# Kernel tuning notes

Measured on AMD Instinct MI355X. Metric: run time of the kernel, lower is better.

The kernel has to match this reference:

```python
import jax, jax.numpy as jnp
import numpy as np
import math

N_EMBD = 512
N_BRANCH = 4
BLOCK = 2048
B, T = 2, 2048


def make_rope_tables(dim, max_len):
    inv_freq = 1.0 / (10000.0 ** (np.arange(0, dim, 2, dtype=np.float32) / dim))
    t = np.arange(max_len, dtype=np.float32)
    freqs = np.einsum('i,j->ij', t, inv_freq)  # [max_len, dim/2]
    return jnp.asarray(np.cos(freqs)), jnp.asarray(np.sin(freqs))


def apply_rope(xq, cos, sin):
    # xq: [..., T, C]; cos/sin: [T, C/2]
    x1 = xq[..., 0::2]
    x2 = xq[..., 1::2]
    y1 = x1 * cos - x2 * sin
    y2 = x1 * sin + x2 * cos
    return jnp.stack((y1, y2), axis=-1).reshape(xq.shape)


def setup_inputs() -> dict:
    key = jax.random.key(0)
    ks = jax.random.split(key, 6)
    C, NB = N_EMBD, N_BRANCH
    s = 1.0 / math.sqrt(C)
    a = jax.random.normal(ks[0], (B, T, C), jnp.float32)
    x = jax.random.normal(ks[1], (B, T, C), jnp.float32)
    Wq = jax.random.normal(ks[2], (C, C * NB), jnp.float32) * s
    Wk = jax.random.normal(ks[3], (C, C), jnp.float32) * s
    Wv = jax.random.normal(ks[4], (C, C * NB), jnp.float32) * s
    Wo = jax.random.normal(ks[5], (C, C), jnp.float32) * s
    cos, sin = make_rope_tables(C, BLOCK)
    return {"a": a, "x": x, "Wq": Wq, "Wk": Wk, "Wv": Wv, "Wo": Wo,
            "cos": cos, "sin": sin}


def reference(a, x, Wq, Wk, Wv, Wo, cos, sin):
    Bb, Tt, C = x.shape
    NB = Wq.shape[1] // C
    cos_t = cos[:Tt]
    sin_t = sin[:Tt]

    q = (a @ Wq).reshape(Bb, Tt, NB, C).transpose(0, 2, 1, 3)  # [B,NB,T,C]
    v = (a @ Wv).reshape(Bb, Tt, NB, C).transpose(0, 2, 1, 3)  # [B,NB,T,C]
    k = (x @ Wk)[:, None, :, :]                                # [B,1,T,C]

    q = apply_rope(q, cos_t, sin_t)
    k = apply_rope(k, cos_t, sin_t)

    att = jnp.einsum('bntc,bosc->bnts', q, k) / math.sqrt(C)   # [B,NB,T,T]
    causal = jnp.tril(jnp.ones((Tt, Tt), bool))                # [T,T]
    att_m = jnp.where(causal, att, -jnp.inf)

    # softmax over branch axis; mask is identical across branches, so compute
    # on unmasked logits and zero-out masked positions (== nan_to_num of
    # softmax over fully -inf columns)
    soft_probs = jnp.where(causal, jax.nn.softmax(att, axis=1), 0.0)

    max_val = jnp.max(soft_probs, axis=1, keepdims=True)
    hard_mask = jax.lax.stop_gradient((soft_probs == max_val).astype(att.dtype))
    route_mask = jax.lax.stop_gradient(hard_mask - soft_probs) + soft_probs

    att_max = jnp.max(att_m, axis=1)                           # [B,T,T]
    attn_probs = jax.nn.softmax(att_max, axis=-1)              # [B,T,T]

    combined = attn_probs[:, None, :, :] * route_mask          # [B,NB,T,T]
    y = jnp.einsum('bnts,bnsc->btc', combined, v)              # [B,T,C]
    return y @ Wo
```

## Files before the change

kernel.cpp:

```cpp
#include <hip/hip_runtime.h>
#include <math.h>


#define B_ 2
#define T_ 2048
#define C_ 512
#define NB_ 4
#define C2_ 1024

typedef unsigned short u16;
typedef unsigned char u8;
using short8 = __attribute__((ext_vector_type(8))) short;
using bf16x8 = __attribute__((ext_vector_type(8))) __bf16;
using f32x4  = __attribute__((ext_vector_type(4))) float;

__device__ __forceinline__ float bf2f(u16 u) {
  union { unsigned int i; float f; } v; v.i = ((unsigned int)u) << 16; return v.f;
}
__device__ __forceinline__ u16 f2bf(float f) {
  union { float f; unsigned int i; } v; v.f = f;
  unsigned int u = v.i;
  return (u16)((u + 0x7fffu + ((u >> 16) & 1u)) >> 16);
}
__device__ __forceinline__ f32x4 mfma16x16x32(short8 a, short8 b, f32x4 c) {
  return __builtin_amdgcn_mfma_f32_16x16x32_bf16(
      __builtin_bit_cast(bf16x8, a), __builtin_bit_cast(bf16x8, b), c, 0, 0, 0);
}
__device__ __forceinline__ void split8(const float* s, uint4& hi, uint4& lo) {
  u16 h[8], l[8];
#pragma unroll
  for (int j = 0; j < 8; ++j) {
    h[j] = f2bf(s[j]);
    l[j] = f2bf(s[j] - bf2f(h[j]));
  }
  hi.x = h[0] | ((unsigned)h[1] << 16); hi.y = h[2] | ((unsigned)h[3] << 16);
  hi.z = h[4] | ((unsigned)h[5] << 16); hi.w = h[6] | ((unsigned)h[7] << 16);
  lo.x = l[0] | ((unsigned)l[1] << 16); lo.y = l[2] | ((unsigned)l[3] << 16);
  lo.z = l[4] | ((unsigned)l[5] << 16); lo.w = l[6] | ((unsigned)l[7] << 16);
}
__device__ __forceinline__ int swz(int row) { return ((row >> 1) & 3) << 3; }

template <int MODE>
__global__ __launch_bounds__(256) void gemm_qk(const float* __restrict__ A,
                                               const float* __restrict__ W,
                                               u16* __restrict__ out,
                                               const float* __restrict__ cosT,
                                               const float* __restrict__ sinT,
                                               const int N, const int K) {
  __shared__ u16 Ah[64][32], Al[64][32];
  __shared__ u16 Bh[64][32], Bl[64][32];
  const int tid = threadIdx.x;
  const int wave = tid >> 6, lane = tid & 63;
  const int m0 = blockIdx.y << 6, n0 = blockIdx.x << 6;
  const f32x4 zero = {0.f, 0.f, 0.f, 0.f};
  f32x4 acc[4] = {zero, zero, zero, zero};
  const int srow = tid >> 2, koff = ((tid & 3) << 3) ^ swz(tid >> 2);
  const int lrow = lane & 15, lk = ((lane >> 4) << 3) ^ swz(lane & 15);
  for (int kk = 0; kk < K; kk += 32) {
    const int kg = (tid & 3) << 3;
    float av[8];
    *(float4*)(av) = *(const float4*)(&A[(size_t)(m0 + srow) * K + kk + kg]);
    *(float4*)(av + 4) =
        *(const float4*)(&A[(size_t)(m0 + srow) * K + kk + kg + 4]);
    uint4 hi, lo;
    split8(av, hi, lo);
    *(uint4*)(&Ah[srow][koff]) = hi;
    *(uint4*)(&Al[srow][koff]) = lo;
    float wv[8];
#pragma unroll
    for (int j = 0; j < 8; ++j)
      wv[j] = W[(size_t)(kk + kg + j) * N + n0 + srow];
    split8(wv, hi, lo);
    *(uint4*)(&Bh[srow][koff]) = hi;
    *(uint4*)(&Bl[srow][koff]) = lo;
    __syncthreads();
    short8 ah = *(const short8*)(&Ah[(wave << 4) + lrow][lk]);
    short8 al = *(const short8*)(&Al[(wave << 4) + lrow][lk]);
#pragma unroll
    for (int ns = 0; ns < 4; ++ns) {
      short8 bh = *(const short8*)(&Bh[(ns << 4) + lrow][lk]);
      short8 bl = *(const short8*)(&Bl[(ns << 4) + lrow][lk]);
      acc[ns] = mfma16x16x32(ah, bh, acc[ns]);
      acc[ns] = mfma16x16x32(al, bh, acc[ns]);
      acc[ns] = mfma16x16x32(ah, bl, acc[ns]);
    }
    __syncthreads();
  }
  const int r0 = m0 + (wave << 4) + ((lane >> 4) << 2);
  const int cb = n0 + (lane & 15);
#pragma unroll
  for (int ns = 0; ns < 4; ++ns) {
#pragma unroll
    for (int r = 0; r < 4; ++r) {
      const int rg = r0 + r;
      const int cg = cb + (ns << 4);
      float v = acc[ns][r];
      float pv = __shfl_xor(v, 1);
      const int t = rg & (T_ - 1);
      const int c = (MODE == 1) ? (cg & (C_ - 1)) : cg;
      const int i = c >> 1;
      const float cf = cosT[(t << 8) + i];
      const float sf = sinT[(t << 8) + i];
      float x1 = (lane & 1) ? pv : v;
      float x2 = (lane & 1) ? v : pv;
      float y = (lane & 1) ? (x1 * sf + x2 * cf) : (x1 * cf - x2 * sf);
      if (MODE == 1) y *= 0.044194173824159216f;
      const u16 hi = f2bf(y);
      const u16 lo = f2bf(y - bf2f(hi));
      size_t rowoff;
      if (MODE == 1) {
        const int b = rg >> 11, n = cg >> 9;
        rowoff = ((size_t)((b * NB_ + n) * T_ + t)) * C2_;
      } else {
        rowoff = (size_t)rg * C2_;
      }
      out[rowoff + c] = hi;
      out[rowoff + C_ + c] = lo;
    }
  }
}

template <int AF32, int OF32>
__global__ __launch_bounds__(256) void gemm_hi(const void* __restrict__ Ap,
                                               const float* __restrict__ W,
                                               void* __restrict__ outp,
                                               const int N, const int K) {
  __shared__ u16 As[64][32];
  __shared__ u16 Bs[64][32];
  const int tid = threadIdx.x;
  const int wave = tid >> 6, lane = tid & 63;
  const int m0 = blockIdx.y << 6, n0 = blockIdx.x << 6;
  const f32x4 zero = {0.f, 0.f, 0.f, 0.f};
  f32x4 acc[4] = {zero, zero, zero, zero};
  const int srow = tid >> 2, koff = ((tid & 3) << 3) ^ swz(tid >> 2);
  const int lrow = lane & 15, lk = ((lane >> 4) << 3) ^ swz(lane & 15);
  for (int kk = 0; kk < K; kk += 32) {
    const int kg = (tid & 3) << 3;
    if (AF32) {
      const float* A = (const float*)Ap;
      float av[8];
      *(float4*)(av) = *(const float4*)(&A[(size_t)(m0 + srow) * K + kk + kg]);
      *(float4*)(av + 4) =
          *(const float4*)(&A[(size_t)(m0 + srow) * K + kk + kg + 4]);
      uint4 hi;
      hi.x = f2bf(av[0]) | ((unsigned)f2bf(av[1]) << 16);
      hi.y = f2bf(av[2]) | ((unsigned)f2bf(av[3]) << 16);
      hi.z = f2bf(av[4]) | ((unsigned)f2bf(av[5]) << 16);
      hi.w = f2bf(av[6]) | ((unsigned)f2bf(av[7]) << 16);
      *(uint4*)(&As[srow][koff]) = hi;
    } else {
      const u16* A = (const u16*)Ap;
      *(uint4*)(&As[srow][koff]) =
          *(const uint4*)(&A[(size_t)(m0 + srow) * K + kk + kg]);
    }
    uint4 hi;
    {
      float w[8];
#pragma unroll
      for (int j = 0; j < 8; ++j)
        w[j] = W[(size_t)(kk + kg + j) * N + n0 + srow];
      hi.x = f2bf(w[0]) | ((unsigned)f2bf(w[1]) << 16);
      hi.y = f2bf(w[2]) | ((unsigned)f2bf(w[3]) << 16);
      hi.z = f2bf(w[4]) | ((unsigned)f2bf(w[5]) << 16);
      hi.w = f2bf(w[6]) | ((unsigned)f2bf(w[7]) << 16);
    }
    *(uint4*)(&Bs[srow][koff]) = hi;
    __syncthreads();
    short8 af = *(const short8*)(&As[(wave << 4) + lrow][lk]);
#pragma unroll
    for (int ns = 0; ns < 4; ++ns) {
      short8 bf = *(const short8*)(&Bs[(ns << 4) + lrow][lk]);
      acc[ns] = mfma16x16x32(af, bf, acc[ns]);
    }
    __syncthreads();
  }
  const int r0 = m0 + (wave << 4) + ((lane >> 4) << 2);
  const int cb = n0 + (lane & 15);
#pragma unroll
  for (int ns = 0; ns < 4; ++ns) {
#pragma unroll
    for (int r = 0; r < 4; ++r) {
      const size_t idx = (size_t)(r0 + r) * N + cb + (ns << 4);
      if (OF32) ((float*)outp)[idx] = acc[ns][r];
      else ((u16*)outp)[idx] = f2bf(acc[ns][r]);
    }
  }
}

__global__ __launch_bounds__(256) void transpose_v_k(const u16* __restrict__ Vraw,
                                                     u16* __restrict__ VT) {
  const int bid = blockIdx.x;
  const int ct = bid & 7;
  const int ttile = (bid >> 3) & 31;
  const int n = (bid >> 8) & 3;
  const int b = bid >> 10;
  __shared__ u16 tile[64][68];
  const int tid = threadIdx.x;
  const int rr = tid >> 4;
  const int cc = (tid & 15) << 2;
  const int t0 = ttile << 6, c0 = ct << 6;
#pragma unroll
  for (int it = 0; it < 4; ++it) {
    const int r = (it << 4) + rr;
    *(ushort4*)(&tile[r][cc]) = *(const ushort4*)(
        &Vraw[((size_t)((b << 11) + t0 + r)) * (NB_ * C_) + n * C_ + c0 + cc]);
  }
  __syncthreads();
#pragma unroll
  for (int it = 0; it < 4; ++it) {
    const int c = (it << 4) + rr;
    ushort4 w;
    w.x = tile[cc + 0][c]; w.y = tile[cc + 1][c];
    w.z = tile[cc + 2][c]; w.w = tile[cc + 3][c];
    *(ushort4*)(&VT[((size_t)((b * NB_ + n) * C_ + c0 + c)) * T_ + t0 + cc]) = w;
  }
}

__global__ __launch_bounds__(256) void scores_k(const u16* __restrict__ Qcat,
                                                const u16* __restrict__ Kcat,
                                                u16* __restrict__ Mout,
                                                u8* __restrict__ Mask) {
  const int tri = blockIdx.x;
  int tt = (int)((sqrtf(8.f * (float)tri + 1.f) - 1.f) * 0.5f);
  while ((tt + 1) * (tt + 2) / 2 <= tri) ++tt;
  while (tt * (tt + 1) / 2 > tri) --tt;
  const int ss = tri - tt * (tt + 1) / 2;
  const int b = blockIdx.y;
  __shared__ u16 Qh[NB_][64][32], Ql[NB_][64][32];
  __shared__ u16 Kh[64][32], Kl[64][32];
  const int tid = threadIdx.x;
  const int wave = tid >> 6, lane = tid & 63;
  const int t0 = tt << 6, s0 = ss << 6;
  const f32x4 zero = {0.f, 0.f, 0.f, 0.f};
  f32x4 acc[NB_][4];
  for (int n = 0; n < NB_; ++n)
    for (int j = 0; j < 4; ++j) acc[n][j] = zero;
  const int srow = tid >> 2, koff = ((tid & 3) << 3) ^ swz(tid >> 2);
  const int lrow = lane & 15, lk = ((lane >> 4) << 3) ^ swz(lane & 15);
  const int kg = (tid & 3) << 3;
  for (int kk = 0; kk < C_; kk += 32) {
#pragma unroll
    for (int n = 0; n < NB_; ++n) {
      const size_t qb =
          ((size_t)((b * NB_ + n) * T_ + t0 + srow)) * C2_ + kk + kg;
      *(uint4*)(&Qh[n][srow][koff]) = *(const uint4*)(&Qcat[qb]);
      *(uint4*)(&Ql[n][srow][koff]) = *(const uint4*)(&Qcat[qb + C_]);
    }
    const size_t kb = ((size_t)((b << 11) + s0 + srow)) * C2_ + kk + kg;
    *(uint4*)(&Kh[srow][koff]) = *(const uint4*)(&Kcat[kb]);
    *(uint4*)(&Kl[srow][koff]) = *(const uint4*)(&Kcat[kb + C_]);
    __syncthreads();
    short8 qh[NB_], ql[NB_];
#pragma unroll
    for (int n = 0; n < NB_; ++n) {
      qh[n] = *(const short8*)(&Qh[n][(wave << 4) + lrow][lk]);
      ql[n] = *(const short8*)(&Ql[n][(wave << 4) + lrow][lk]);
    }
#pragma unroll
    for (int ns = 0; ns < 4; ++ns) {
      short8 kh = *(const short8*)(&Kh[(ns << 4) + lrow][lk]);
      short8 kl = *(const short8*)(&Kl[(ns << 4) + lrow][lk]);
#pragma unroll
      for (int n = 0; n < NB_; ++n) {
        acc[n][ns] = mfma16x16x32(qh[n], kh, acc[n][ns]);
        acc[n][ns] = mfma16x16x32(ql[n], kh, acc[n][ns]);
        acc[n][ns] = mfma16x16x32(qh[n], kl, acc[n][ns]);
      }
    }
    __syncthreads();
  }
  const int tb = t0 + (wave << 4) + ((lane >> 4) << 2);
  const int sb = s0 + (lane & 15);
#pragma unroll
  for (int ns = 0; ns < 4; ++ns) {
#pragma unroll
    for (int r = 0; r < 4; ++r) {
      const int t = tb + r, s = sb + (ns << 4);
      float a0 = acc[0][ns][r], a1 = acc[1][ns][r];
      float a2 = acc[2][ns][r], a3 = acc[3][ns][r];
      float m = fmaxf(fmaxf(a0, a1), fmaxf(a2, a3));
      u8 msk = (u8)((a0 == m) | ((a1 == m) << 1) | ((a2 == m) << 2) |
                    ((a3 == m) << 3));
      if (s > t) { m = -__builtin_inff(); msk = 0; }
      const size_t idx = (size_t)b * T_ * T_ + (size_t)t * T_ + s;
      Mout[idx] = f2bf(m);
      Mask[idx] = msk;
    }
  }
}

__global__ __launch_bounds__(256) void rowstats_k(const u16* __restrict__ Mb,
                                                  float* __restrict__ Rm,
                                                  float* __restrict__ Rz) {
  const int r = (blockIdx.x << 2) + (threadIdx.x >> 6);
  const int lane = threadIdx.x & 63;
  const int b = r >> 11, t = r & (T_ - 1);
  const u16* row = Mb + (size_t)b * T_ * T_ + (size_t)t * T_;
  float m = -__builtin_inff();
  for (int s = lane; s <= t; s += 64) m = fmaxf(m, bf2f(row[s]));
#pragma unroll
  for (int off = 32; off; off >>= 1) m = fmaxf(m, __shfl_xor(m, off));
  float z = 0.f;
  for (int s = lane; s <= t; s += 64) z += expf(bf2f(row[s]) - m);
#pragma unroll
  for (int off = 32; off; off >>= 1) z += __shfl_xor(z, off);
  if (lane == 0) { Rm[r] = m; Rz[r] = 1.f / z; }
}

__global__ __launch_bounds__(256) void pbuild_k(const u16* __restrict__ Mb,
                                                const float* __restrict__ Rm,
                                                const float* __restrict__ Rz,
                                                u16* __restrict__ Pb) {
  const int r = blockIdx.x;
  const float rm = Rm[r], rz = Rz[r];
  const size_t off = ((size_t)r << 11) + (threadIdx.x << 3);
  ushort4 m0 = *(const ushort4*)(&Mb[off]);
  ushort4 m1 = *(const ushort4*)(&Mb[off + 4]);
  u16 o[8];
  o[0] = f2bf(expf(bf2f(m0.x) - rm) * rz);
  o[1] = f2bf(expf(bf2f(m0.y) - rm) * rz);
  o[2] = f2bf(expf(bf2f(m0.z) - rm) * rz);
  o[3] = f2bf(expf(bf2f(m0.w) - rm) * rz);
  o[4] = f2bf(expf(bf2f(m1.x) - rm) * rz);
  o[5] = f2bf(expf(bf2f(m1.y) - rm) * rz);
  o[6] = f2bf(expf(bf2f(m1.z) - rm) * rz);
  o[7] = f2bf(expf(bf2f(m1.w) - rm) * rz);
  uint4 w;
  w.x = o[0] | ((unsigned)o[1] << 16); w.y = o[2] | ((unsigned)o[3] << 16);
  w.z = o[4] | ((unsigned)o[5] << 16); w.w = o[6] | ((unsigned)o[7] << 16);
  *(uint4*)(&Pb[off]) = w;
}

__global__ __launch_bounds__(256) void pv_k(const u16* __restrict__ Pb,
                                            const u8* __restrict__ Mask,
                                            const u16* __restrict__ VT,
                                            u16* __restrict__ Y) {
  const int ypair = blockIdx.x, cblk = blockIdx.y, b = blockIdx.z;
  const int c0 = cblk << 5;
  __shared__ u16 Ps[NB_][64][32];
  __shared__ u16 Vs[NB_][32][32];
  const int tid = threadIdx.x;
  const int wave = tid >> 6, lane = tid & 63;
  const int prow = tid >> 2, soff = (tid & 3) << 3;
  const int psoff = soff ^ swz(prow);
  const int vrow = tid >> 3, vsoff = (tid & 7) << 2;
  const int vcol = ((((tid & 7) >> 1) ^ ((vrow >> 1) & 3)) << 3) |
                   ((tid & 1) << 2);
  const int lrow = lane & 15, lk = ((lane >> 4) << 3) ^ swz(lane & 15);
  const f32x4 zero = {0.f, 0.f, 0.f, 0.f};
  const size_t vrow_base[NB_] = {
      ((size_t)((b * NB_ + 0) * C_ + c0 + vrow)) * T_,
      ((size_t)((b * NB_ + 1) * C_ + c0 + vrow)) * T_,
      ((size_t)((b * NB_ + 2) * C_ + c0 + vrow)) * T_,
      ((size_t)((b * NB_ + 3) * C_ + c0 + vrow)) * T_};

  for (int half = 0; half < 2; ++half) {
    const int tt = half ? (31 - ypair) : ypair;
    const int t0 = tt << 6;
    const int nchunk = (tt + 1) << 1;
    const size_t pro = ((size_t)((b << 11) + t0 + prow)) << 11;
    f32x4 acc[2] = {zero, zero};
    uint4 pu; uint2 mk2; uint2 vv[NB_];
    pu = *(const uint4*)(&Pb[pro + soff]);
    mk2 = *(const uint2*)(&Mask[pro + soff]);
#pragma unroll
    for (int n = 0; n < NB_; ++n)
      vv[n] = *(const uint2*)(&VT[vrow_base[n] + vsoff]);
    for (int ck = 0; ck < nchunk; ++ck) {
      u16 p[8] = {(u16)pu.x, (u16)(pu.x >> 16), (u16)pu.y, (u16)(pu.y >> 16),
                  (u16)pu.z, (u16)(pu.z >> 16), (u16)pu.w, (u16)(pu.w >> 16)};
      u8 mk[8] = {(u8)mk2.x, (u8)(mk2.x >> 8), (u8)(mk2.x >> 16),
                  (u8)(mk2.x >> 24), (u8)mk2.y, (u8)(mk2.y >> 8),
                  (u8)(mk2.y >> 16), (u8)(mk2.y >> 24)};
#pragma unroll
      for (int n = 0; n < NB_; ++n) {
        uint4 wv;
        wv.x = (unsigned)(((mk[0] >> n) & 1) ? p[0] : 0) |
               ((unsigned)(((mk[1] >> n) & 1) ? p[1] : 0) << 16);
        wv.y = (unsigned)(((mk[2] >> n) & 1) ? p[2] : 0) |
               ((unsigned)(((mk[3] >> n) & 1) ? p[3] : 0) << 16);
        wv.z = (unsigned)(((mk[4] >> n) & 1) ? p[4] : 0) |
               ((unsigned)(((mk[5] >> n) & 1) ? p[5] : 0) << 16);
        wv.w = (unsigned)(((mk[6] >> n) & 1) ? p[6] : 0) |
               ((unsigned)(((mk[7] >> n) & 1) ? p[7] : 0) << 16);
        *(uint4*)(&Ps[n][prow][psoff]) = wv;
        *(uint2*)(&Vs[n][vrow][vcol]) = vv[n];
      }
      __syncthreads();
      if (ck + 1 < nchunk) {
        const int sB = (ck + 1) << 5;
        pu = *(const uint4*)(&Pb[pro + sB + soff]);
        mk2 = *(const uint2*)(&Mask[pro + sB + soff]);
#pragma unroll
        for (int n = 0; n < NB_; ++n)
          vv[n] = *(const uint2*)(&VT[vrow_base[n] + sB + vsoff]);
      }
#pragma unroll
      for (int n = 0; n < NB_; ++n) {
        short8 af = *(const short8*)(&Ps[n][(wave << 4) + lrow][lk]);
#pragma unroll
        for (int cs = 0; cs < 2; ++cs) {
          short8 bf = *(const short8*)(&Vs[n][(cs << 4) + lrow][lk]);
          acc[cs] = mfma16x16x32(af, bf, acc[cs]);
        }
      }
      __syncthreads();
    }
    const int tb = t0 + (wave << 4) + ((lane >> 4) << 2);
    const int cbs = c0 + (lane & 15);
#pragma unroll
    for (int cs = 0; cs < 2; ++cs) {
#pragma unroll
      for (int r = 0; r < 4; ++r) {
        Y[(size_t)((b << 11) + tb + r) * C_ + cbs + (cs << 4)] =
            f2bf(acc[cs][r]);
      }
    }
  }
}

extern "C" void kernel_launch(void* const* d_in, const int* in_sizes, int n_in,
                              void* d_out, int out_size, void* d_ws,
                              size_t ws_size, hipStream_t stream) {
  (void)in_sizes; (void)n_in; (void)out_size; (void)ws_size;
  const float* a    = (const float*)d_in[0];
  const float* x    = (const float*)d_in[1];
  const float* Wq   = (const float*)d_in[2];
  const float* Wk   = (const float*)d_in[3];
  const float* Wv   = (const float*)d_in[4];
  const float* Wo   = (const float*)d_in[5];
  const float* cosT = (const float*)d_in[6];
  const float* sinT = (const float*)d_in[7];

  char* w = (char*)d_ws;
  u16* Qcat   = (u16*)(w + 0);
  u16* Kcat   = (u16*)(w + 33554432);
  u16* Vraw   = (u16*)(w + 41943040);
  u16* VT     = (u16*)(w + 58720256);
  u8*  Mask   = (u8*)(w + 75497472);
  float* Rm   = (float*)(w + 83886080);
  float* Rz   = (float*)(w + 83902464);
  u16* Pb     = (u16*)(w + 83918848);
  u16* Mb     = Vraw;
  u16* Y      = Qcat;

  const dim3 blk(256);
  gemm_qk<1><<<dim3(32, 64), blk, 0, stream>>>(a, Wq, Qcat, cosT, sinT, 2048, 512);
  gemm_qk<2><<<dim3(8, 64), blk, 0, stream>>>(x, Wk, Kcat, cosT, sinT, 512, 512);
  gemm_hi<1, 0><<<dim3(32, 64), blk, 0, stream>>>(a, Wv, (void*)Vraw, 2048, 512);
  transpose_v_k<<<dim3(2048), blk, 0, stream>>>(Vraw, VT);
  scores_k<<<dim3(528, 2), blk, 0, stream>>>(Qcat, Kcat, Mb, Mask);
  rowstats_k<<<dim3(1024), blk, 0, stream>>>(Mb, Rm, Rz);
  pbuild_k<<<dim3(4096), blk, 0, stream>>>(Mb, Rm, Rz, Pb);
  pv_k<<<dim3(16, 16, 2), blk, 0, stream>>>(Pb, Mask, VT, Y);
  gemm_hi<0, 1><<<dim3(8, 64), blk, 0, stream>>>(Y, Wo, d_out, 512, 512);
}
```

Before: 393.8 us.

## Double-buffer scores_k LDS tiles with async global_load_lds prefetch

Replaces register-staged global-to-LDS copies in the scores kernel with direct global_load_lds transfers into double-buffered shared-memory tiles. The next K-slice is prefetched while the current one feeds the MFMAs, using explicit vmcnt waits and raw barriers. The XOR swizzle on LDS rows is dropped because the direct LDS load writes a fixed lane-contiguous layout, which can bring back LDS bank conflicts on the fragment reads. LDS use doubles, which may lower occupancy.

```diff
diff --git a/kernel.cpp b/kernel.cpp
--- a/kernel.cpp
+++ b/kernel.cpp
@@ -226,8 +226,8 @@
   while (tt * (tt + 1) / 2 > tri) --tt;
   const int ss = tri - tt * (tt + 1) / 2;
   const int b = blockIdx.y;
-  __shared__ u16 Qh[NB_][64][32], Ql[NB_][64][32];
-  __shared__ u16 Kh[64][32], Kl[64][32];
+  __shared__ __align__(16) u16 Qh[2][NB_][64][32], Ql[2][NB_][64][32];
+  __shared__ __align__(16) u16 Kh[2][64][32], Kl[2][64][32];
   const int tid = threadIdx.x;
   const int wave = tid >> 6, lane = tid & 63;
   const int t0 = tt << 6, s0 = ss << 6;
@@ -235,31 +235,55 @@
   f32x4 acc[NB_][4];
   for (int n = 0; n < NB_; ++n)
     for (int j = 0; j < 4; ++j) acc[n][j] = zero;
-  const int srow = tid >> 2, koff = ((tid & 3) << 3) ^ swz(tid >> 2);
-  const int lrow = lane & 15, lk = ((lane >> 4) << 3) ^ swz(lane & 15);
-  const int kg = (tid & 3) << 3;
+  const int srow = tid >> 2, kg = (tid & 3) << 3;
+  const int lrow = lane & 15, lk = (lane >> 4) << 3;
+  const int wrow = wave << 4;
+  const size_t qstride = (size_t)T_ * C2_;
+  const size_t qbase = ((size_t)(b * NB_ * T_ + t0 + srow)) * C2_ + kg;
+  const size_t kbase = ((size_t)((b << 11) + s0 + srow)) * C2_ + kg;
+
+  auto stage_sc = [&](int d, int kko) {
+#pragma unroll
+    for (int n = 0; n < NB_; ++n) {
+      const size_t qb = qbase + (size_t)n * qstride + kko;
+      __builtin_amdgcn_global_load_lds(
+          (const __attribute__((address_space(1))) void*)&Qcat[qb],
+          (__attribute__((address_space(3))) void*)&Qh[d][n][wrow][0], 16, 0, 0);
+      __builtin_amdgcn_global_load_lds(
+          (const __attribute__((address_space(1))) void*)&Qcat[qb + C_],
+          (__attribute__((address_space(3))) void*)&Ql[d][n][wrow][0], 16, 0, 0);
+    }
+    __builtin_amdgcn_global_load_lds(
+        (const __attribute__((address_space(1))) void*)&Kcat[kbase + kko],
+        (__attribute__((address_space(3))) void*)&Kh[d][wrow][0], 16, 0, 0);
+    __builtin_amdgcn_global_load_lds(
+        (const __attribute__((address_space(1))) void*)&Kcat[kbase + kko + C_],
+        (__attribute__((address_space(3))) void*)&Kl[d][wrow][0], 16, 0, 0);
+  };
+
+  stage_sc(0, 0);
+  int cur = 0;
+#pragma unroll 2
   for (int kk = 0; kk < C_; kk += 32) {
+    if (kk + 32 < C_) {
+      stage_sc(cur ^ 1, kk + 32);
+      asm volatile("s_waitcnt vmcnt(10)" ::: "memory");
+    } else {
+      asm volatile("s_waitcnt vmcnt(0)" ::: "memory");
+    }
+    __builtin_amdgcn_sched_barrier(0);
+    __builtin_amdgcn_s_barrier();
+    __builtin_amdgcn_sched_barrier(0);
+    short8 qh[NB_], ql[NB_];
 #pragma unroll
     for (int n = 0; n < NB_; ++n) {
-      const size_t qb =
-          ((size_t)((b * NB_ + n) * T_ + t0 + srow)) * C2_ + kk + kg;
-      *(uint4*)(&Qh[n][srow][koff]) = *(const uint4*)(&Qcat[qb]);
-      *(uint4*)(&Ql[n][srow][koff]) = *(const uint4*)(&Qcat[qb + C_]);
-    }
-    const size_t kb = ((size_t)((b << 11) + s0 + srow)) * C2_ + kk + kg;
-    *(uint4*)(&Kh[srow][koff]) = *(const uint4*)(&Kcat[kb]);
-    *(uint4*)(&Kl[srow][koff]) = *(const uint4*)(&Kcat[kb + C_]);
-    __syncthreads();
-    short8 qh[NB_], ql[NB_];
-#pragma unroll
-    for (int n = 0; n < NB_; ++n) {
-      qh[n] = *(const short8*)(&Qh[n][(wave << 4) + lrow][lk]);
-      ql[n] = *(const short8*)(&Ql[n][(wave << 4) + lrow][lk]);
+      qh[n] = *(const short8*)(&Qh[cur][n][wrow + lrow][lk]);
+      ql[n] = *(const short8*)(&Ql[cur][n][wrow + lrow][lk]);
     }
 #pragma unroll
     for (int ns = 0; ns < 4; ++ns) {
-      short8 kh = *(const short8*)(&Kh[(ns << 4) + lrow][lk]);
-      short8 kl = *(const short8*)(&Kl[(ns << 4) + lrow][lk]);
+      short8 kh = *(const short8*)(&Kh[cur][(ns << 4) + lrow][lk]);
+      short8 kl = *(const short8*)(&Kl[cur][(ns << 4) + lrow][lk]);
 #pragma unroll
       for (int n = 0; n < NB_; ++n) {
         acc[n][ns] = mfma16x16x32(qh[n], kh, acc[n][ns]);
@@ -267,7 +291,11 @@
         acc[n][ns] = mfma16x16x32(qh[n], kl, acc[n][ns]);
       }
     }
-    __syncthreads();
+    __builtin_amdgcn_sched_barrier(0);
+    asm volatile("" ::: "memory");
+    __builtin_amdgcn_s_barrier();
+    __builtin_amdgcn_sched_barrier(0);
+    cur ^= 1;
   }
   const int tb = t0 + (wave << 4) + ((lane >> 4) << 2);
   const int sb = s0 + (lane & 15);
```

Result: faster. 378.8 us (-3.8%).

## Fuse softmax probability build into PV kernel and remap score tile order

Applied to the files above, without the earlier changes.

Removes the separate pbuild_k pass by computing exp(m - rowmax) * rinv on the fly inside pv_k from the bf16 max-logit matrix and row stats. This avoids writing and rereading a full T×T bf16 probability buffer per batch and saves one launch. The cost is that the exps are recomputed redundantly across the 16 column blocks of pv_k. Separately, scores_k's block-to-triangle mapping is permuted (interleaving by 8 with stride 66) to spread heavy and light tiles across the scheduler.

```diff
diff --git a/kernel.cpp b/kernel.cpp
--- a/kernel.cpp
+++ b/kernel.cpp
@@ -220,7 +220,7 @@
                                                 const u16* __restrict__ Kcat,
                                                 u16* __restrict__ Mout,
                                                 u8* __restrict__ Mask) {
-  const int tri = blockIdx.x;
+  const int tri = ((blockIdx.x & 7) * 66) + (blockIdx.x >> 3);
   int tt = (int)((sqrtf(8.f * (float)tri + 1.f) - 1.f) * 0.5f);
   while ((tt + 1) * (tt + 2) / 2 <= tri) ++tt;
   while (tt * (tt + 1) / 2 > tri) --tt;
@@ -307,31 +307,9 @@
   if (lane == 0) { Rm[r] = m; Rz[r] = 1.f / z; }
 }
 
-__global__ __launch_bounds__(256) void pbuild_k(const u16* __restrict__ Mb,
-                                                const float* __restrict__ Rm,
-                                                const float* __restrict__ Rz,
-                                                u16* __restrict__ Pb) {
-  const int r = blockIdx.x;
-  const float rm = Rm[r], rz = Rz[r];
-  const size_t off = ((size_t)r << 11) + (threadIdx.x << 3);
-  ushort4 m0 = *(const ushort4*)(&Mb[off]);
-  ushort4 m1 = *(const ushort4*)(&Mb[off + 4]);
-  u16 o[8];
-  o[0] = f2bf(expf(bf2f(m0.x) - rm) * rz);
-  o[1] = f2bf(expf(bf2f(m0.y) - rm) * rz);
-  o[2] = f2bf(expf(bf2f(m0.z) - rm) * rz);
-  o[3] = f2bf(expf(bf2f(m0.w) - rm) * rz);
-  o[4] = f2bf(expf(bf2f(m1.x) - rm) * rz);
-  o[5] = f2bf(expf(bf2f(m1.y) - rm) * rz);
-  o[6] = f2bf(expf(bf2f(m1.z) - rm) * rz);
-  o[7] = f2bf(expf(bf2f(m1.w) - rm) * rz);
-  uint4 w;
-  w.x = o[0] | ((unsigned)o[1] << 16); w.y = o[2] | ((unsigned)o[3] << 16);
-  w.z = o[4] | ((unsigned)o[5] << 16); w.w = o[6] | ((unsigned)o[7] << 16);
-  *(uint4*)(&Pb[off]) = w;
-}
-
-__global__ __launch_bounds__(256) void pv_k(const u16* __restrict__ Pb,
+__global__ __launch_bounds__(256) void pv_k(const u16* __restrict__ Mb,
+                                            const float* __restrict__ Rm,
+                                            const float* __restrict__ Rz,
                                             const u8* __restrict__ Mask,
                                             const u16* __restrict__ VT,
                                             u16* __restrict__ Y) {
@@ -358,17 +336,23 @@
     const int tt = half ? (31 - ypair) : ypair;
     const int t0 = tt << 6;
     const int nchunk = (tt + 1) << 1;
-    const size_t pro = ((size_t)((b << 11) + t0 + prow)) << 11;
+    const int rg = (b << 11) + t0 + prow;
+    const size_t pro = (size_t)rg << 11;
+    const float rm = Rm[rg], rz = Rz[rg];
     f32x4 acc[2] = {zero, zero};
     uint4 pu; uint2 mk2; uint2 vv[NB_];
-    pu = *(const uint4*)(&Pb[pro + soff]);
+    pu = *(const uint4*)(&Mb[pro + soff]);
     mk2 = *(const uint2*)(&Mask[pro + soff]);
 #pragma unroll
     for (int n = 0; n < NB_; ++n)
       vv[n] = *(const uint2*)(&VT[vrow_base[n] + vsoff]);
     for (int ck = 0; ck < nchunk; ++ck) {
-      u16 p[8] = {(u16)pu.x, (u16)(pu.x >> 16), (u16)pu.y, (u16)(pu.y >> 16),
-                  (u16)pu.z, (u16)(pu.z >> 16), (u16)pu.w, (u16)(pu.w >> 16)};
+      u16 m8[8] = {(u16)pu.x, (u16)(pu.x >> 16), (u16)pu.y, (u16)(pu.y >> 16),
+                   (u16)pu.z, (u16)(pu.z >> 16), (u16)pu.w, (u16)(pu.w >> 16)};
+      u16 p[8];
+#pragma unroll
+      for (int j = 0; j < 8; ++j)
+        p[j] = f2bf(expf(bf2f(m8[j]) - rm) * rz);
       u8 mk[8] = {(u8)mk2.x, (u8)(mk2.x >> 8), (u8)(mk2.x >> 16),
                   (u8)(mk2.x >> 24), (u8)mk2.y, (u8)(mk2.y >> 8),
                   (u8)(mk2.y >> 16), (u8)(mk2.y >> 24)};
@@ -389,7 +373,7 @@
       __syncthreads();
       if (ck + 1 < nchunk) {
         const int sB = (ck + 1) << 5;
-        pu = *(const uint4*)(&Pb[pro + sB + soff]);
+        pu = *(const uint4*)(&Mb[pro + sB + soff]);
         mk2 = *(const uint2*)(&Mask[pro + sB + soff]);
 #pragma unroll
         for (int n = 0; n < NB_; ++n)
@@ -440,7 +424,6 @@
   u8*  Mask   = (u8*)(w + 75497472);
   float* Rm   = (float*)(w + 83886080);
   float* Rz   = (float*)(w + 83902464);
-  u16* Pb     = (u16*)(w + 83918848);
   u16* Mb     = Vraw;
   u16* Y      = Qcat;
 
@@ -451,7 +434,6 @@
   transpose_v_k<<<dim3(2048), blk, 0, stream>>>(Vraw, VT);
   scores_k<<<dim3(528, 2), blk, 0, stream>>>(Qcat, Kcat, Mb, Mask);
   rowstats_k<<<dim3(1024), blk, 0, stream>>>(Mb, Rm, Rz);
-  pbuild_k<<<dim3(4096), blk, 0, stream>>>(Mb, Rm, Rz, Pb);
-  pv_k<<<dim3(16, 16, 2), blk, 0, stream>>>(Pb, Mask, VT, Y);
+  pv_k<<<dim3(16, 16, 2), blk, 0, stream>>>(Mb, Rm, Rz, Mask, VT, Y);
   gemm_hi<0, 1><<<dim3(8, 64), blk, 0, stream>>>(Y, Wo, d_out, 512, 512);
 }
```

Measured after the change: 384.4 us. 1.02x faster.
